# Performance work log

Measured on AMD Instinct MI355X. Metric: run time of the kernel, lower is better.

Reference implementation:

```python
import jax, jax.numpy as jnp
import numpy as np

DIM_K = 64
DIM_V = 64
MODEL_DIM = 1024


def setup_inputs() -> dict:
    key = jax.random.key(0)
    ks = jax.random.split(key, 9)
    B, T, C = 4, 4096, MODEL_DIM
    scale = 1.0 / np.sqrt(C)
    return {
        "Q": jax.random.normal(ks[0], (B, T, C), dtype=jnp.float32),
        "K": jax.random.normal(ks[1], (B, T, C), dtype=jnp.float32),
        "V": jax.random.normal(ks[2], (B, T, C), dtype=jnp.float32),
        "Wq": jax.random.normal(ks[3], (C, DIM_K), dtype=jnp.float32) * scale,
        "bq": jax.random.normal(ks[4], (DIM_K,), dtype=jnp.float32) * 0.02,
        "Wk": jax.random.normal(ks[5], (C, DIM_K), dtype=jnp.float32) * scale,
        "bk": jax.random.normal(ks[6], (DIM_K,), dtype=jnp.float32) * 0.02,
        "Wv": jax.random.normal(ks[7], (C, DIM_V), dtype=jnp.float32) * scale,
        "bv": jax.random.normal(ks[8], (DIM_V,), dtype=jnp.float32) * 0.02,
    }


def reference(Q, K, V, Wq, bq, Wk, bk, Wv, bv):
    # Linear projections: [B,T,C] @ [C,dk] -> [B,T,dk]
    q = jnp.einsum("btc,cd->btd", Q, Wq) + bq
    k = jnp.einsum("btc,cd->btd", K, Wk) + bk
    v = jnp.einsum("btc,cd->btd", V, Wv) + bv
    T = q.shape[1]
    # Scaled dot-product scores [B,T,T], causal mask, softmax (dropout p=0 -> identity)
    scores = jnp.einsum("bqd,bkd->bqk", q, k) / jnp.sqrt(jnp.float32(DIM_K))
    causal = jnp.tril(jnp.ones((T, T), dtype=bool))
    scores = jnp.where(causal, scores, -jnp.inf)
    weights = jax.nn.softmax(scores, axis=-1)
    return jnp.einsum("bqk,bkd->bqd", weights, v)
```

## Files before the change

### kernel.cpp

```cpp
#include <hip/hip_runtime.h>
#include <hip/hip_bf16.h>
#include <cstdint>
#include <cstddef>


typedef __attribute__((ext_vector_type(8))) short short8;
typedef __attribute__((ext_vector_type(4))) float f32x4;
typedef __attribute__((ext_vector_type(4))) unsigned int uint4v;
typedef __attribute__((ext_vector_type(4))) unsigned short ushort4v;
typedef unsigned short ushort;

#define MFMA16x16x32(A,B,C) __builtin_amdgcn_mfma_f32_16x16x32_bf16((A),(B),(C),0,0,0)

static __device__ __forceinline__ unsigned pack2_bf16(float f0, float f1){
  unsigned u0 = __builtin_bit_cast(unsigned, f0) + 0x8000u;
  unsigned u1 = __builtin_bit_cast(unsigned, f1) + 0x8000u;
  return __builtin_amdgcn_perm(u1, u0, 0x07060302u);
}
static __device__ __forceinline__ unsigned short bf16u(float f){
  return (unsigned short)((__builtin_bit_cast(unsigned, f) + 0x8000u) >> 16);
}
static __device__ __forceinline__ short8 cvt8(f32x4 a, f32x4 b){
  union { unsigned u[4]; short8 s; } r;
  r.u[0] = pack2_bf16(a[0], a[1]);
  r.u[1] = pack2_bf16(a[2], a[3]);
  r.u[2] = pack2_bf16(b[0], b[1]);
  r.u[3] = pack2_bf16(b[2], b[3]);
  return r.s;
}
static __device__ __forceinline__ float fast_exp2(float x){
  float r; asm("v_exp_f32 %0, %1" : "=v"(r) : "v"(x)); return r;
}
static __device__ __forceinline__ float fast_rcp(float x){
  float r; asm("v_rcp_f32 %0, %1" : "=v"(r) : "v"(x)); return r;
}
static __device__ __forceinline__ void gl_lds16(const void* g, void* l){
  __builtin_amdgcn_global_load_lds(
      (const __attribute__((address_space(1))) void*)g,
      (__attribute__((address_space(3))) void*)l, 16, 0, 0);
}

__global__ __launch_bounds__(256) void pack_w(
    const float* __restrict__ Wq, const float* __restrict__ Wk,
    const float* __restrict__ Wv, unsigned short* __restrict__ Wp,
    float* __restrict__ out, float* __restrict__ Lbuf)
{
  int t = blockIdx.x * 256 + threadIdx.x;
  if (t < 24576){
    int lane = t & 63, nf = (t >> 6) & 3, cc = (t >> 8) & 31, p = t >> 13;
    int qd = lane >> 4, l = lane & 15;
    const float* W = (p == 0) ? Wq : ((p == 1) ? Wk : Wv);
    const float* src = W + (size_t)(cc * 32 + qd * 8) * 64 + nf * 16 + l;
    uint4v u;
    #pragma unroll
    for (int j = 0; j < 4; ++j)
      u[j] = pack2_bf16(src[(2 * j) * 64], src[(2 * j + 1) * 64]);
    *(uint4v*)(Wp + (size_t)t * 8) = u;
  }
  const f32x4 z = (f32x4){0.f, 0.f, 0.f, 0.f};
  f32x4* o4 = (f32x4*)out;
  f32x4* l4 = (f32x4*)Lbuf;
  for (int i = t; i < 262144 + 4096; i += 65536){
    if (i < 262144) o4[i] = z;
    else l4[i - 262144] = z;
  }
}

__global__ __launch_bounds__(512, 6) void proj_gemm(
    const float* __restrict__ Qx, const float* __restrict__ Kx, const float* __restrict__ Vx,
    const float* __restrict__ bqp, const float* __restrict__ bkp, const float* __restrict__ bvp,
    const unsigned short* __restrict__ Wp,
    unsigned short* __restrict__ qb, unsigned short* __restrict__ kb,
    unsigned short* __restrict__ vt)
{
  __shared__ float cs[4][64][16];

  const int tid = threadIdx.x;
  const int lane = tid & 63, wid = tid >> 6;
  const int kh = wid & 1, rt = wid >> 1;
  const int qd = lane >> 4, l = lane & 15;
  const int p = blockIdx.y;
  const float* X = (p == 0) ? Qx : ((p == 1) ? Kx : Vx);
  const float* bias = (p == 0) ? bqp : ((p == 1) ? bkp : bvp);
  const unsigned short* W = Wp + (size_t)p * 65536;

  const int row0 = blockIdx.x * 64 + rt * 16;
  const float* xa = X + (size_t)(row0 + l) * 1024 + qd * 8;
  const unsigned short* wb = W + (size_t)lane * 8;

  f32x4 acc[4];
  #pragma unroll
  for (int nf = 0; nf < 4; ++nf) acc[nf] = (f32x4){0.f, 0.f, 0.f, 0.f};

  const int cc0 = kh * 16;
  #pragma unroll 4
  for (int cc = cc0; cc < cc0 + 16; ++cc){
    f32x4 al = *(const f32x4*)(xa + cc * 32);
    f32x4 ah = *(const f32x4*)(xa + cc * 32 + 4);
    const unsigned short* wc = wb + (size_t)cc * 2048;
    short8 b0 = *(const short8*)(wc);
    short8 b1 = *(const short8*)(wc + 512);
    short8 b2 = *(const short8*)(wc + 1024);
    short8 b3 = *(const short8*)(wc + 1536);
    short8 a = cvt8(al, ah);
    acc[0] = MFMA16x16x32(a, b0, acc[0]);
    acc[1] = MFMA16x16x32(a, b1, acc[1]);
    acc[2] = MFMA16x16x32(a, b2, acc[2]);
    acc[3] = MFMA16x16x32(a, b3, acc[3]);
  }

  if (kh == 1){
    float* dst = &cs[rt][lane][0];
    #pragma unroll
    for (int nf = 0; nf < 4; ++nf)
      *(f32x4*)(dst + nf * 4) = acc[nf];
  }
  __syncthreads();
  if (kh == 0){
    const float* src = &cs[rt][lane][0];
    #pragma unroll
    for (int nf = 0; nf < 4; ++nf){
      f32x4 o = *(const f32x4*)(src + nf * 4);
      acc[nf][0] += o[0]; acc[nf][1] += o[1];
      acc[nf][2] += o[2]; acc[nf][3] += o[3];
    }

    if (p == 2){
      int tg = row0 + qd * 4;
      int b = tg >> 12, tl = tg & 4095;
      #pragma unroll
      for (int nf = 0; nf < 4; ++nf){
        float bb = bias[nf * 16 + l];
        ushort4v pk;
        #pragma unroll
        for (int r = 0; r < 4; ++r) pk[r] = bf16u(acc[nf][r] + bb);
        *(ushort4v*)(vt + ((size_t)b * 64 + nf * 16 + l) * 4096 + tl) = pk;
      }
    } else {
      unsigned short* o = (p == 0) ? qb : kb;
      #pragma unroll
      for (int nf = 0; nf < 4; ++nf){
        float bb = bias[nf * 16 + l];
        #pragma unroll
        for (int r = 0; r < 4; ++r){
          int row = row0 + qd * 4 + r;
          o[(size_t)row * 64 + nf * 16 + l] = bf16u(acc[nf][r] + bb);
        }
      }
    }
  }
}

#define K1 0.18033688011112042f

__global__ __launch_bounds__(256) void flash_split(
    const ushort* __restrict__ qb, const ushort* __restrict__ kb,
    const ushort* __restrict__ vt, float* __restrict__ out,
    float* __restrict__ Lbuf)
{
  __shared__ ushort Ks0[4096];
  __shared__ ushort Ks1[4096];
  __shared__ ushort Vs0[4096];
  __shared__ ushort Vs1[4096];
  __shared__ ushort pbuf[4][16 * 40];

  const int tid = threadIdx.x;
  const int lane = tid & 63, wid = tid >> 6;
  const int qd = lane >> 4, l = lane & 15;
  const int lw = l & 7;

  int bidx = (int)blockIdx.x;
  const int batch = bidx & 3;
  int j = 287 - (bidx >> 2);
  int g = 0;
  while (j >= 4 * (g + 1) * (g + 2)) ++g;
  int j2 = j - 4 * g * (g + 1);
  int tq = j2 / (g + 1);
  int s = j2 - tq * (g + 1);
  const int q0b = (8 * g + tq) * 64;
  const int kvstart = s * 512;
  const int kvend = min(kvstart + 512, q0b + 64);
  const int q0w = q0b + wid * 16;

  const ushort* kbB = kb + (size_t)batch * 262144;
  const ushort* vtB = vt + (size_t)batch * 262144;

  const ushort* qrow = qb + ((size_t)(batch * 4096 + q0w + l)) * 64 + qd * 8;
  short8 Qf0 = *(const short8*)(qrow);
  short8 Qf1 = *(const short8*)(qrow + 32);

  const f32x4 Zc = (f32x4){0.f, 0.f, 0.f, 0.f};
  f32x4 Oc[4] = {Zc, Zc, Zc, Zc};
  f32x4 Lacc = Zc;
  short8 onesf;
  #pragma unroll
  for (int i = 0; i < 8; ++i) onesf[i] = (short)0x3F80;

  ushort* pw = &pbuf[wid][0];
  ushort* pwr = pw + qd * 160 + l;
  const ushort* prd = pw + l * 40 + qd * 8;

#define STAGE(KA, VA, KVC) do{                                                 \
    int r8_ = lane >> 3, sw_ = ((lane & 7) ^ r8_) << 3;                        \
    int rA_ = wid * 8 + r8_;                                                   \
    const ushort* gk_ = kbB + (size_t)((KVC) + rA_) * 64 + sw_;                \
    gl_lds16(gk_,            &(KA)[wid * 512]);                                \
    gl_lds16(gk_ + 32 * 64,  &(KA)[2048 + wid * 512]);                         \
    const ushort* gv_ = vtB + (size_t)rA_ * 4096 + (KVC) + sw_;                \
    gl_lds16(gv_,              &(VA)[wid * 512]);                              \
    gl_lds16(gv_ + 32 * 4096,  &(VA)[2048 + wid * 512]);                       \
  } while (0)

#define CHUNK(KA, VA, ROFF, KVG) do{                                           \
    if ((KVG) < q0w + 16){                                                     \
      const ushort* KsB_ = &(KA)[0];                                           \
      const ushort* VsB_ = &(VA)[0];                                           \
      short8 k0_ = *(const short8*)(KsB_ + (l + (ROFF)) * 64 + ((qd ^ lw) << 3));        \
      short8 k1_ = *(const short8*)(KsB_ + (l + (ROFF)) * 64 + (((qd + 4) ^ lw) << 3));  \
      short8 k2_ = *(const short8*)(KsB_ + (l + 16 + (ROFF)) * 64 + ((qd ^ lw) << 3));   \
      short8 k3_ = *(const short8*)(KsB_ + (l + 16 + (ROFF)) * 64 + (((qd + 4) ^ lw) << 3)); \
      f32x4 s0_ = MFMA16x16x32(Qf0, k0_, Zc);                                  \
      s0_ = MFMA16x16x32(Qf1, k1_, s0_);                                       \
      f32x4 s1_ = MFMA16x16x32(Qf0, k2_, Zc);                                  \
      s1_ = MFMA16x16x32(Qf1, k3_, s1_);                                       \
      float p0_[4], p1_[4];                                                    \
      _Pragma("unroll")                                                        \
      for (int r = 0; r < 4; ++r){                                             \
        p0_[r] = fast_exp2(s0_[r] * K1);                                       \
        p1_[r] = fast_exp2(s1_[r] * K1);                                       \
      }                                                                        \
      if ((KVG) + 31 > q0w){                                                   \
        _Pragma("unroll")                                                      \
        for (int r = 0; r < 4; ++r){                                           \
          int q_ = q0w + qd * 4 + r;                                           \
          if ((KVG) + l > q_) p0_[r] = 0.f;                                    \
          if ((KVG) + 16 + l > q_) p1_[r] = 0.f;                               \
        }                                                                      \
      }                                                                        \
      _Pragma("unroll")                                                        \
      for (int r = 0; r < 4; ++r){                                             \
        pwr[r * 40] = bf16u(p0_[r]);                                           \
        pwr[r * 40 + 16] = bf16u(p1_[r]);                                      \
      }                                                                        \
      short8 Pf_ = *(const short8*)(prd);                                      \
      int vs_ = ((qd + ((ROFF) >> 3)) ^ lw) << 3;                              \
      short8 v0_ = *(const short8*)(VsB_ + (l     ) * 64 + vs_);               \
      short8 v1_ = *(const short8*)(VsB_ + (l + 16) * 64 + vs_);               \
      short8 v2_ = *(const short8*)(VsB_ + (l + 32) * 64 + vs_);               \
      short8 v3_ = *(const short8*)(VsB_ + (l + 48) * 64 + vs_);               \
      Lacc = MFMA16x16x32(Pf_, onesf, Lacc);                                   \
      Oc[0] = MFMA16x16x32(Pf_, v0_, Oc[0]);                                   \
      Oc[1] = MFMA16x16x32(Pf_, v1_, Oc[1]);                                   \
      Oc[2] = MFMA16x16x32(Pf_, v2_, Oc[2]);                                   \
      Oc[3] = MFMA16x16x32(Pf_, v3_, Oc[3]);                                   \
    }                                                                          \
  } while (0)

  const int nst = (kvend - kvstart) >> 6;
  int kvc = kvstart;
  STAGE(Ks0, Vs0, kvc);
  __syncthreads();
  int it = 0;
  for (; it + 2 <= nst; it += 2){
    STAGE(Ks1, Vs1, kvc + 64);
    CHUNK(Ks0, Vs0, 0, kvc);
    CHUNK(Ks0, Vs0, 32, kvc + 32);
    __syncthreads();
    if (it + 2 < nst) STAGE(Ks0, Vs0, kvc + 128);
    CHUNK(Ks1, Vs1, 0, kvc + 64);
    CHUNK(Ks1, Vs1, 32, kvc + 96);
    __syncthreads();
    kvc += 128;
  }
  if (it < nst){
    CHUNK(Ks0, Vs0, 0, kvc);
    CHUNK(Ks0, Vs0, 32, kvc + 32);
  }
#undef STAGE
#undef CHUNK

  float* ob = out + ((size_t)(batch * 4096 + q0w + qd * 4)) * 64 + l;
  #pragma unroll
  for (int nf = 0; nf < 4; ++nf)
    #pragma unroll
    for (int r = 0; r < 4; ++r)
      atomicAdd(&ob[(size_t)r * 64 + nf * 16], Oc[nf][r]);
  if (l == 0){
    float* lb = Lbuf + batch * 4096 + q0w + qd * 4;
    #pragma unroll
    for (int r = 0; r < 4; ++r) atomicAdd(&lb[r], Lacc[r]);
  }
}

__global__ __launch_bounds__(256) void normalize(
    float* __restrict__ out, const float* __restrict__ Lbuf)
{
  int idx = blockIdx.x * 256 + threadIdx.x;
  f32x4 v = ((f32x4*)out)[idx];
  float inv = fast_rcp(Lbuf[idx >> 4]);
  v[0] *= inv; v[1] *= inv; v[2] *= inv; v[3] *= inv;
  ((f32x4*)out)[idx] = v;
}

extern "C" void kernel_launch(void* const* d_in, const int* in_sizes, int n_in,
                              void* d_out, int out_size, void* d_ws, size_t ws_size,
                              hipStream_t stream)
{
  const float* Q  = (const float*)d_in[0];
  const float* K  = (const float*)d_in[1];
  const float* V  = (const float*)d_in[2];
  const float* Wq = (const float*)d_in[3];
  const float* bq = (const float*)d_in[4];
  const float* Wk = (const float*)d_in[5];
  const float* bk = (const float*)d_in[6];
  const float* Wv = (const float*)d_in[7];
  const float* bv = (const float*)d_in[8];
  float* out = (float*)d_out;

  unsigned short* qb   = (unsigned short*)d_ws;
  unsigned short* kbuf = qb + (size_t)16384 * 64;
  unsigned short* vtp  = kbuf + (size_t)16384 * 64;
  unsigned short* Wp   = vtp + (size_t)16384 * 64;
  float* Lbuf = (float*)(Wp + (size_t)3 * 65536);

  pack_w<<<256, 256, 0, stream>>>(Wq, Wk, Wv, Wp, out, Lbuf);
  proj_gemm<<<dim3(256, 3), 512, 0, stream>>>(Q, K, V, bq, bk, bv, Wp, qb, kbuf, vtp);
  flash_split<<<1152, 256, 0, stream>>>(qb, kbuf, vtp, out, Lbuf);
  normalize<<<1024, 256, 0, stream>>>(out, Lbuf);
}
```

Before: 249.2 us.

## Stage projection input tiles through LDS with double-buffered async global-to-LDS loads

The projection GEMM now stages each 32-row block of fp32 activations into XOR-swizzled LDS buffers using global-to-LDS copies, double-buffered across four K phases, instead of each wave loading its strided rows directly from global memory. Blocks shrink to 32 rows with a four-way K split across waves (reduced through LDS), doubling the grid. This aims to get coalesced, overlapped reads of the large fp32 inputs, at the cost of 64KB of LDS per block, lower occupancy and extra barriers and reduction work.

```diff
diff --git a/kernel.cpp b/kernel.cpp
--- a/kernel.cpp
+++ b/kernel.cpp
@@ -66,65 +66,99 @@
   }
 }
 
-__global__ __launch_bounds__(512, 6) void proj_gemm(
+__global__ __launch_bounds__(512, 4) void proj_gemm(
     const float* __restrict__ Qx, const float* __restrict__ Kx, const float* __restrict__ Vx,
     const float* __restrict__ bqp, const float* __restrict__ bkp, const float* __restrict__ bvp,
     const unsigned short* __restrict__ Wp,
     unsigned short* __restrict__ qb, unsigned short* __restrict__ kb,
     unsigned short* __restrict__ vt)
 {
-  __shared__ float cs[4][64][16];
+  __shared__ float P0[8192];
+  __shared__ float P1[8192];
 
   const int tid = threadIdx.x;
   const int lane = tid & 63, wid = tid >> 6;
-  const int kh = wid & 1, rt = wid >> 1;
+  const int kq = wid & 3, rt = wid >> 2;
   const int qd = lane >> 4, l = lane & 15;
+  const int cw = l & 7;
   const int p = blockIdx.y;
   const float* X = (p == 0) ? Qx : ((p == 1) ? Kx : Vx);
   const float* bias = (p == 0) ? bqp : ((p == 1) ? bkp : bvp);
   const unsigned short* W = Wp + (size_t)p * 65536;
 
-  const int row0 = blockIdx.x * 64 + rt * 16;
-  const float* xa = X + (size_t)(row0 + l) * 1024 + qd * 8;
+  const int row0b = blockIdx.x * 32;
+  const float* Xblk = X + (size_t)row0b * 1024;
   const unsigned short* wb = W + (size_t)lane * 8;
 
   f32x4 acc[4];
   #pragma unroll
   for (int nf = 0; nf < 4; ++nf) acc[nf] = (f32x4){0.f, 0.f, 0.f, 0.f};
 
-  const int cc0 = kh * 16;
-  #pragma unroll 4
-  for (int cc = cc0; cc < cc0 + 16; ++cc){
-    f32x4 al = *(const f32x4*)(xa + cc * 32);
-    f32x4 ah = *(const f32x4*)(xa + cc * 32 + 4);
-    const unsigned short* wc = wb + (size_t)cc * 2048;
-    short8 b0 = *(const short8*)(wc);
-    short8 b1 = *(const short8*)(wc + 512);
-    short8 b2 = *(const short8*)(wc + 1024);
-    short8 b3 = *(const short8*)(wc + 1536);
-    short8 a = cvt8(al, ah);
-    acc[0] = MFMA16x16x32(a, b0, acc[0]);
-    acc[1] = MFMA16x16x32(a, b1, acc[1]);
-    acc[2] = MFMA16x16x32(a, b2, acc[2]);
-    acc[3] = MFMA16x16x32(a, b3, acc[3]);
-  }
-
-  if (kh == 1){
-    float* dst = &cs[rt][lane][0];
+#define STAGEP(PB, PP) do{                                                     \
+    _Pragma("unroll")                                                          \
+    for (int r_ = 0; r_ < 4; ++r_){                                            \
+      int rr_ = wid * 4 + r_;                                                  \
+      const float* src_ = Xblk + (size_t)rr_ * 1024 + (PP) * 256               \
+                          + ((lane ^ (rr_ & 7)) << 2);                         \
+      gl_lds16(src_, (PB) + rr_ * 256);                                        \
+    }                                                                          \
+  } while (0)
+
+#define PCOMPP(PB, PP) do{                                                     \
+    _Pragma("unroll")                                                          \
+    for (int i_ = 0; i_ < 2; ++i_){                                            \
+      int lc_ = kq * 2 + i_;                                                   \
+      int cc_ = (PP) * 8 + lc_;                                                \
+      const unsigned short* wc_ = wb + (size_t)cc_ * 2048;                     \
+      short8 b0_ = *(const short8*)(wc_);                                      \
+      short8 b1_ = *(const short8*)(wc_ + 512);                                \
+      short8 b2_ = *(const short8*)(wc_ + 1024);                               \
+      short8 b3_ = *(const short8*)(wc_ + 1536);                               \
+      const float* rb_ = (PB) + (rt * 16 + l) * 256;                           \
+      int s_ = lc_ * 8 + qd * 2;                                               \
+      f32x4 al_ = *(const f32x4*)(rb_ + ((s_ ^ cw) << 2));                     \
+      f32x4 ah_ = *(const f32x4*)(rb_ + (((s_ + 1) ^ cw) << 2));               \
+      short8 a_ = cvt8(al_, ah_);                                              \
+      acc[0] = MFMA16x16x32(a_, b0_, acc[0]);                                  \
+      acc[1] = MFMA16x16x32(a_, b1_, acc[1]);                                  \
+      acc[2] = MFMA16x16x32(a_, b2_, acc[2]);                                  \
+      acc[3] = MFMA16x16x32(a_, b3_, acc[3]);                                  \
+    }                                                                          \
+  } while (0)
+
+  STAGEP(P0, 0);
+  __syncthreads();
+  #pragma unroll
+  for (int pp = 0; pp < 4; ++pp){
+    const float* cur = (pp & 1) ? P1 : P0;
+    float* nxt = (pp & 1) ? P0 : P1;
+    if (pp < 3) STAGEP(nxt, pp + 1);
+    PCOMPP(cur, pp);
+    __syncthreads();
+  }
+#undef STAGEP
+#undef PCOMPP
+
+  if (kq != 0){
+    float* dst = P0 + ((size_t)(rt * 3 + (kq - 1)) * 64 + lane) * 16;
     #pragma unroll
     for (int nf = 0; nf < 4; ++nf)
       *(f32x4*)(dst + nf * 4) = acc[nf];
   }
   __syncthreads();
-  if (kh == 0){
-    const float* src = &cs[rt][lane][0];
-    #pragma unroll
-    for (int nf = 0; nf < 4; ++nf){
-      f32x4 o = *(const f32x4*)(src + nf * 4);
-      acc[nf][0] += o[0]; acc[nf][1] += o[1];
-      acc[nf][2] += o[2]; acc[nf][3] += o[3];
+  if (kq == 0){
+    #pragma unroll
+    for (int j = 0; j < 3; ++j){
+      const float* src = P0 + ((size_t)(rt * 3 + j) * 64 + lane) * 16;
+      #pragma unroll
+      for (int nf = 0; nf < 4; ++nf){
+        f32x4 o = *(const f32x4*)(src + nf * 4);
+        acc[nf][0] += o[0]; acc[nf][1] += o[1];
+        acc[nf][2] += o[2]; acc[nf][3] += o[3];
+      }
     }
 
+    const int row0 = row0b + rt * 16;
     if (p == 2){
       int tg = row0 + qd * 4;
       int b = tg >> 12, tl = tg & 4095;
@@ -324,7 +358,7 @@
   float* Lbuf = (float*)(Wp + (size_t)3 * 65536);
 
   pack_w<<<256, 256, 0, stream>>>(Wq, Wk, Wv, Wp, out, Lbuf);
-  proj_gemm<<<dim3(256, 3), 512, 0, stream>>>(Q, K, V, bq, bk, bv, Wp, qb, kbuf, vtp);
+  proj_gemm<<<dim3(512, 3), 512, 0, stream>>>(Q, K, V, bq, bk, bv, Wp, qb, kbuf, vtp);
   flash_split<<<1152, 256, 0, stream>>>(qb, kbuf, vtp, out, Lbuf);
   normalize<<<1024, 256, 0, stream>>>(out, Lbuf);
 }
```

Result: no change. 248.1 us (-0.4%).

## Split projection into Q/K launches and an 8-way K-split V projection

Applied to the files above, without the earlier changes.

The fused three-way projection launch becomes two launches of a Q/K kernel plus a dedicated V kernel. The V kernel handles 16 rows per block and splits the 1024-wide reduction across 8 waves, each preloading its weight slice into registers, then reduces the partial sums through shared memory before writing the transposed V output. The aim is more blocks and more memory-level parallelism for the V projection and its transposed stores. The cost is two extra kernel launches and more shared-memory reduction traffic.

```diff
diff --git a/kernel.cpp b/kernel.cpp
--- a/kernel.cpp
+++ b/kernel.cpp
@@ -66,12 +66,10 @@
   }
 }
 
-__global__ __launch_bounds__(512, 6) void proj_gemm(
-    const float* __restrict__ Qx, const float* __restrict__ Kx, const float* __restrict__ Vx,
-    const float* __restrict__ bqp, const float* __restrict__ bkp, const float* __restrict__ bvp,
-    const unsigned short* __restrict__ Wp,
-    unsigned short* __restrict__ qb, unsigned short* __restrict__ kb,
-    unsigned short* __restrict__ vt)
+__global__ __launch_bounds__(512, 6) void proj_qk(
+    const float* __restrict__ X, const float* __restrict__ bias,
+    const unsigned short* __restrict__ W,
+    unsigned short* __restrict__ o)
 {
   __shared__ float cs[4][64][16];
 
@@ -79,10 +77,6 @@
   const int lane = tid & 63, wid = tid >> 6;
   const int kh = wid & 1, rt = wid >> 1;
   const int qd = lane >> 4, l = lane & 15;
-  const int p = blockIdx.y;
-  const float* X = (p == 0) ? Qx : ((p == 1) ? Kx : Vx);
-  const float* bias = (p == 0) ? bqp : ((p == 1) ? bkp : bvp);
-  const unsigned short* W = Wp + (size_t)p * 65536;
 
   const int row0 = blockIdx.x * 64 + rt * 16;
   const float* xa = X + (size_t)(row0 + l) * 1024 + qd * 8;
@@ -120,33 +114,117 @@
     const float* src = &cs[rt][lane][0];
     #pragma unroll
     for (int nf = 0; nf < 4; ++nf){
-      f32x4 o = *(const f32x4*)(src + nf * 4);
-      acc[nf][0] += o[0]; acc[nf][1] += o[1];
-      acc[nf][2] += o[2]; acc[nf][3] += o[3];
+      f32x4 ov = *(const f32x4*)(src + nf * 4);
+      acc[nf][0] += ov[0]; acc[nf][1] += ov[1];
+      acc[nf][2] += ov[2]; acc[nf][3] += ov[3];
     }
-
-    if (p == 2){
-      int tg = row0 + qd * 4;
-      int b = tg >> 12, tl = tg & 4095;
+    #pragma unroll
+    for (int nf = 0; nf < 4; ++nf){
+      float bb = bias[nf * 16 + l];
+      #pragma unroll
+      for (int r = 0; r < 4; ++r){
+        int row = row0 + qd * 4 + r;
+        o[(size_t)row * 64 + nf * 16 + l] = bf16u(acc[nf][r] + bb);
+      }
+    }
+  }
+}
+
+__global__ __launch_bounds__(512, 4) void proj_v8(
+    const float* __restrict__ X, const float* __restrict__ bias,
+    const unsigned short* __restrict__ Wp,
+    unsigned short* __restrict__ vt)
+{
+  __shared__ float cs[7][64][16];
+
+  const int tid = threadIdx.x;
+  const int lane = tid & 63, ks = tid >> 6;
+  const int qd = lane >> 4, l = lane & 15;
+  const unsigned short* W = Wp + (size_t)2 * 65536;
+
+  const int row0 = blockIdx.x * 16;
+  const float* xa = X + (size_t)(row0 + l) * 1024 + qd * 8 + (size_t)(ks * 4) * 32;
+  const unsigned short* wb = W + (size_t)lane * 8 + (size_t)(ks * 4) * 2048;
+
+  short8 w00, w01, w02, w03, w10, w11, w12, w13;
+  short8 w20, w21, w22, w23, w30, w31, w32, w33;
+  {
+    const unsigned short* wc = wb;
+    w00 = *(const short8*)(wc);        w01 = *(const short8*)(wc + 512);
+    w02 = *(const short8*)(wc + 1024); w03 = *(const short8*)(wc + 1536);
+    wc = wb + 2048;
+    w10 = *(const short8*)(wc);        w11 = *(const short8*)(wc + 512);
+    w12 = *(const short8*)(wc + 1024); w13 = *(const short8*)(wc + 1536);
+    wc = wb + 4096;
+    w20 = *(const short8*)(wc);        w21 = *(const short8*)(wc + 512);
+    w22 = *(const short8*)(wc + 1024); w23 = *(const short8*)(wc + 1536);
+    wc = wb + 6144;
+    w30 = *(const short8*)(wc);        w31 = *(const short8*)(wc + 512);
+    w32 = *(const short8*)(wc + 1024); w33 = *(const short8*)(wc + 1536);
+  }
+
+  f32x4 acc[4];
+  #pragma unroll
+  for (int nf = 0; nf < 4; ++nf) acc[nf] = (f32x4){0.f, 0.f, 0.f, 0.f};
+
+  {
+    f32x4 a0l = *(const f32x4*)(xa);
+    f32x4 a0h = *(const f32x4*)(xa + 4);
+    f32x4 a1l = *(const f32x4*)(xa + 32);
+    f32x4 a1h = *(const f32x4*)(xa + 36);
+    f32x4 a2l = *(const f32x4*)(xa + 64);
+    f32x4 a2h = *(const f32x4*)(xa + 68);
+    f32x4 a3l = *(const f32x4*)(xa + 96);
+    f32x4 a3h = *(const f32x4*)(xa + 100);
+    short8 a0 = cvt8(a0l, a0h);
+    acc[0] = MFMA16x16x32(a0, w00, acc[0]);
+    acc[1] = MFMA16x16x32(a0, w01, acc[1]);
+    acc[2] = MFMA16x16x32(a0, w02, acc[2]);
+    acc[3] = MFMA16x16x32(a0, w03, acc[3]);
+    short8 a1 = cvt8(a1l, a1h);
+    acc[0] = MFMA16x16x32(a1, w10, acc[0]);
+    acc[1] = MFMA16x16x32(a1, w11, acc[1]);
+    acc[2] = MFMA16x16x32(a1, w12, acc[2]);
+    acc[3] = MFMA16x16x32(a1, w13, acc[3]);
+    short8 a2 = cvt8(a2l, a2h);
+    acc[0] = MFMA16x16x32(a2, w20, acc[0]);
+    acc[1] = MFMA16x16x32(a2, w21, acc[1]);
+    acc[2] = MFMA16x16x32(a2, w22, acc[2]);
+    acc[3] = MFMA16x16x32(a2, w23, acc[3]);
+    short8 a3 = cvt8(a3l, a3h);
+    acc[0] = MFMA16x16x32(a3, w30, acc[0]);
+    acc[1] = MFMA16x16x32(a3, w31, acc[1]);
+    acc[2] = MFMA16x16x32(a3, w32, acc[2]);
+    acc[3] = MFMA16x16x32(a3, w33, acc[3]);
+  }
+
+  if (ks != 0){
+    float* dst = &cs[ks - 1][lane][0];
+    #pragma unroll
+    for (int nf = 0; nf < 4; ++nf)
+      *(f32x4*)(dst + nf * 4) = acc[nf];
+  }
+  __syncthreads();
+  if (ks == 0){
+    #pragma unroll
+    for (int j = 0; j < 7; ++j){
+      const float* src = &cs[j][lane][0];
       #pragma unroll
       for (int nf = 0; nf < 4; ++nf){
-        float bb = bias[nf * 16 + l];
-        ushort4v pk;
-        #pragma unroll
-        for (int r = 0; r < 4; ++r) pk[r] = bf16u(acc[nf][r] + bb);
-        *(ushort4v*)(vt + ((size_t)b * 64 + nf * 16 + l) * 4096 + tl) = pk;
+        f32x4 ov = *(const f32x4*)(src + nf * 4);
+        acc[nf][0] += ov[0]; acc[nf][1] += ov[1];
+        acc[nf][2] += ov[2]; acc[nf][3] += ov[3];
       }
-    } else {
-      unsigned short* o = (p == 0) ? qb : kb;
+    }
+    int tg = row0 + qd * 4;
+    int b = tg >> 12, tl = tg & 4095;
+    #pragma unroll
+    for (int nf = 0; nf < 4; ++nf){
+      float bb = bias[nf * 16 + l];
+      ushort4v pk;
       #pragma unroll
-      for (int nf = 0; nf < 4; ++nf){
-        float bb = bias[nf * 16 + l];
-        #pragma unroll
-        for (int r = 0; r < 4; ++r){
-          int row = row0 + qd * 4 + r;
-          o[(size_t)row * 64 + nf * 16 + l] = bf16u(acc[nf][r] + bb);
-        }
-      }
+      for (int r = 0; r < 4; ++r) pk[r] = bf16u(acc[nf][r] + bb);
+      *(ushort4v*)(vt + ((size_t)b * 64 + nf * 16 + l) * 4096 + tl) = pk;
     }
   }
 }
@@ -324,7 +402,9 @@
   float* Lbuf = (float*)(Wp + (size_t)3 * 65536);
 
   pack_w<<<256, 256, 0, stream>>>(Wq, Wk, Wv, Wp, out, Lbuf);
-  proj_gemm<<<dim3(256, 3), 512, 0, stream>>>(Q, K, V, bq, bk, bv, Wp, qb, kbuf, vtp);
+  proj_qk<<<256, 512, 0, stream>>>(Q, bq, Wp, qb);
+  proj_qk<<<256, 512, 0, stream>>>(K, bk, Wp + 65536, kbuf);
+  proj_v8<<<1024, 512, 0, stream>>>(V, bv, Wp, vtp);
   flash_split<<<1152, 256, 0, stream>>>(qb, kbuf, vtp, out, Lbuf);
   normalize<<<1024, 256, 0, stream>>>(out, Lbuf);
 }
```

Result: slower. 270.1 us (+8.4%).
